# Kernel optimization log

Measured on AMD Instinct MI355X. Metric: run time of the kernel, lower is better.

Reference implementation:

```python
import jax, jax.numpy as jnp
import numpy as np

N_NODES = 10000

def _gcn_norm(edges, n_nodes):
    # PyG GCNConv default: add self-loops, symmetric normalization D^-1/2 A_hat D^-1/2
    src, dst = edges[0], edges[1]
    loop = jnp.arange(n_nodes, dtype=src.dtype)
    src = jnp.concatenate([src, loop])
    dst = jnp.concatenate([dst, loop])
    deg = jax.ops.segment_sum(jnp.ones_like(dst, dtype=jnp.float32), dst, num_segments=n_nodes)
    dinv = jnp.where(deg > 0, jax.lax.rsqrt(deg), 0.0)
    norm = dinv[src] * dinv[dst]  # [E + N]
    return src, dst, norm

def _gcn_layer(x, src, dst, norm, W, b):
    # linear transform, then gather -> weight -> scatter-add aggregation
    x = x @ W  # [N, F]
    msg = x[src] * norm[:, None]  # [E+N, F]
    out = jax.ops.segment_sum(msg, dst, num_segments=x.shape[0])
    return out + b

def setup_inputs() -> dict:
    key = jax.random.key(0)
    k1, k2, k3, k4 = jax.random.split(key, 4)
    d = 128
    E = 640000
    scale = 1.0 / np.sqrt(d)
    return {
        "nodes_embeddings": jax.random.normal(k1, (N_NODES, d), dtype=jnp.float32),
        "edges": jax.random.randint(k2, (2, E), 0, N_NODES, dtype=jnp.int64),
        "W1": jax.random.normal(k3, (d, d), dtype=jnp.float32) * scale,
        "b1": jnp.zeros((d,), dtype=jnp.float32),
        "W2": jax.random.normal(k4, (d, d), dtype=jnp.float32) * scale,
        "b2": jnp.zeros((d,), dtype=jnp.float32),
    }

def reference(nodes_embeddings, edges, W1, b1, W2, b2):
    src, dst, norm = _gcn_norm(edges, nodes_embeddings.shape[0])
    x = _gcn_layer(nodes_embeddings, src, dst, norm, W1, b1)
    x = _gcn_layer(x, src, dst, norm, W2, b2)
    return x
```

## Files before the change

kernel.cpp:

```cpp
#include <hip/hip_runtime.h>
#include <hip/hip_bf16.h>

#define D 128
#define NBINS 157
#define BIN_CAP 5120
#define EPB 4096

__device__ __forceinline__ unsigned rne_bf16(float f) {
    unsigned u = __float_as_uint(f);
    return (u + 0x7FFFu + ((u >> 16) & 1u)) >> 16;
}
__device__ __forceinline__ float bf16_lo(unsigned u) { return __uint_as_float(u << 16); }
__device__ __forceinline__ float bf16_hi(unsigned u) { return __uint_as_float(u & 0xFFFF0000u); }

__global__ __launch_bounds__(512) void fused_gemm_scatter(
        const float* __restrict__ X, const float* __restrict__ W,
        float* __restrict__ Y,
        const int* __restrict__ src, const int* __restrict__ dst,
        int* __restrict__ binTotal, int* __restrict__ binned,
        int E, int N, int gGemm) {
    __shared__ float smem[D * D];
    int tid = threadIdx.x;

    if ((int)blockIdx.x < gGemm) {
        {
            const float4* W4 = (const float4*)W;
            float4* Ws4 = (float4*)smem;
            #pragma unroll
            for (int i = 0; i < 8; ++i)
                Ws4[tid + 512 * i] = W4[tid + 512 * i];
        }
        __syncthreads();
        const float2* Ws2 = (const float2*)smem;
        int col2 = tid & 63;
        int wv   = __builtin_amdgcn_readfirstlane(tid >> 6);
        int row0 = blockIdx.x * 32 + wv * 4;
        if (row0 >= N) return;

        const float4* xr[4];
        #pragma unroll
        for (int r = 0; r < 4; ++r) {
            int rr = row0 + r; if (rr > N - 1) rr = N - 1;
            xr[r] = (const float4*)(X + (size_t)rr * D);
        }
        float accx[4] = {0.f, 0.f, 0.f, 0.f};
        float accy[4] = {0.f, 0.f, 0.f, 0.f};
        #pragma unroll 8
        for (int kb = 0; kb < 32; ++kb) {
            float4 xv[4];
            #pragma unroll
            for (int r = 0; r < 4; ++r) xv[r] = xr[r][kb];
            #pragma unroll
            for (int kk = 0; kk < 4; ++kk) {
                float2 w = Ws2[(4 * kb + kk) * 64 + col2];
                #pragma unroll
                for (int r = 0; r < 4; ++r) {
                    float xs = ((const float*)&xv[r])[kk];
                    accx[r] = fmaf(xs, w.x, accx[r]);
                    accy[r] = fmaf(xs, w.y, accy[r]);
                }
            }
        }
        #pragma unroll
        for (int r = 0; r < 4; ++r) {
            int rr = row0 + r;
            if (rr < N)
                ((float2*)Y)[(size_t)rr * 64 + col2] = make_float2(accx[r], accy[r]);
        }
    } else {
        int* cnt   = (int*)smem;
        int* loff  = cnt + 160;
        int* gbase = cnt + 320;
        int* scur  = cnt + 480;
        int* stage = cnt + 640;
        for (int b = tid; b < NBINS; b += 512) cnt[b] = 0;
        __syncthreads();

        int bid = blockIdx.x - gGemm;
        int base = bid * EPB + tid * 8;
        int s[8], dl[8], bn[8];
        int ne = 0;
        if (base + 8 <= E) {
            const int4* s4 = (const int4*)(src + base);
            const int4* d4 = (const int4*)(dst + base);
            int4 a0 = s4[0], a1 = s4[1], c0 = d4[0], c1 = d4[1];
            int ss[8] = {a0.x, a0.y, a0.z, a0.w, a1.x, a1.y, a1.z, a1.w};
            int dd[8] = {c0.x, c0.y, c0.z, c0.w, c1.x, c1.y, c1.z, c1.w};
            ne = 8;
            #pragma unroll
            for (int i = 0; i < 8; ++i) { s[i] = ss[i]; bn[i] = dd[i] >> 6; dl[i] = dd[i] & 63; }
        } else {
            for (int i = 0; i < 8; ++i) {
                int e = base + i;
                if (e < E) { s[ne] = src[e]; int d = dst[e]; bn[ne] = d >> 6; dl[ne] = d & 63; ++ne; }
            }
        }
        for (int i = 0; i < ne; ++i) atomicAdd(&cnt[bn[i]], 1);
        __syncthreads();

        if (tid < NBINS) gbase[tid] = atomicAdd(&binTotal[tid], cnt[tid]);
        if (tid < 64) {
            int c0 = (3 * tid     < NBINS) ? cnt[3 * tid    ] : 0;
            int c1 = (3 * tid + 1 < NBINS) ? cnt[3 * tid + 1] : 0;
            int c2 = (3 * tid + 2 < NBINS) ? cnt[3 * tid + 2] : 0;
            int tsum = c0 + c1 + c2;
            int incl = tsum;
            #pragma unroll
            for (int off = 1; off < 64; off <<= 1) {
                int t = __shfl_up(incl, off);
                if (tid >= off) incl += t;
            }
            int excl = incl - tsum;
            if (3 * tid     < NBINS) loff[3 * tid    ] = excl;
            if (3 * tid + 1 < NBINS) loff[3 * tid + 1] = excl + c0;
            if (3 * tid + 2 < NBINS) loff[3 * tid + 2] = excl + c0 + c1;
        }
        __syncthreads();
        if (tid < NBINS) scur[tid] = loff[tid];
        __syncthreads();

        for (int i = 0; i < ne; ++i) {
            int p = atomicAdd(&scur[bn[i]], 1);
            stage[p] = s[i] | (dl[i] << 14);
        }
        __syncthreads();

        int wv = tid >> 6, lane = tid & 63;
        for (int b = wv; b < NBINS; b += 8) {
            int n = cnt[b], so = loff[b], go = b * BIN_CAP + gbase[b];
            for (int i = lane; i < n; i += 64) binned[go + i] = stage[so + i];
        }
    }
}

__global__ __launch_bounds__(256) void sort_bins(const int* __restrict__ binTotal,
                                                 const int* __restrict__ binned,
                                                 unsigned short* __restrict__ csr16,
                                                 float* __restrict__ dinv,
                                                 int* __restrict__ nodeStart,
                                                 int* __restrict__ nodeEnd,
                                                 const float* __restrict__ Y,
                                                 unsigned* __restrict__ Zb,
                                                 unsigned* __restrict__ Zb2, int N) {
    __shared__ int h[4][64];
    __shared__ int cur[4][64];
    __shared__ float sdinv[64];
    __shared__ int padTot;
    __shared__ int stage[BIN_CAP];
    int b = blockIdx.x, tid = threadIdx.x;
    int wv = tid >> 6, lane = tid & 63;
    int cntb = binTotal[b];
    h[wv][lane] = 0;
    __syncthreads();
    const int* bp = binned + b * BIN_CAP;
    for (int i = tid; i < cntb; i += 256) atomicAdd(&h[wv][bp[i] >> 14], 1);
    __syncthreads();
    if (tid < 64) {
        int d0 = h[0][tid], d1 = h[1][tid], d2 = h[2][tid], d3 = h[3][tid];
        int deg = d0 + d1 + d2 + d3;
        int pdeg = (deg + 7) & ~7;
        int incl = pdeg;
        #pragma unroll
        for (int off = 1; off < 64; off <<= 1) {
            int t = __shfl_up(incl, off);
            if (tid >= off) incl += t;
        }
        int excl = incl - pdeg;
        cur[0][tid] = excl;
        cur[1][tid] = excl + d0;
        cur[2][tid] = excl + d0 + d1;
        cur[3][tid] = excl + d0 + d1 + d2;
        float dv = rsqrtf((float)(deg + 1));
        sdinv[tid] = dv;
        if (tid == 63) padTot = incl;
        int node = b * 64 + tid;
        if (node < N) {
            dinv[node]      = dv;
            nodeStart[node] = b * BIN_CAP + excl;
            nodeEnd[node]   = b * BIN_CAP + excl + pdeg;
        }
    }
    __syncthreads();
    int cntPad = padTot;
    for (int i = tid; i < cntPad; i += 256) stage[i] = N;
    __syncthreads();
    for (int i = tid; i < cntb; i += 256) {
        int p = bp[i];
        int pos = atomicAdd(&cur[wv][p >> 14], 1);
        stage[pos] = p & 0x3FFF;
    }
    {
        const float4* Y4 = (const float4*)Y;
        uint2* Zb2v = (uint2*)Zb;
        #pragma unroll
        for (int i = 0; i < 8; ++i) {
            int idx = tid + 256 * i;
            int row = idx >> 5, c = idx & 31;
            int node = b * 64 + row;
            if (node < N) {
                float4 v = Y4[(size_t)node * 32 + c];
                float dv = sdinv[row];
                uint2 o;
                o.x = (rne_bf16(v.y * dv) << 16) | rne_bf16(v.x * dv);
                o.y = (rne_bf16(v.w * dv) << 16) | rne_bf16(v.z * dv);
                Zb2v[(size_t)node * 32 + c] = o;
            }
        }
    }
    if (b == 0 && tid < 64) {
        Zb [(size_t)N * 64 + tid] = 0u;
        Zb2[(size_t)N * 64 + tid] = 0u;
    }
    __syncthreads();
    unsigned short* bw = csr16 + b * BIN_CAP;
    for (int i = tid; i < cntPad; i += 256) bw[i] = (unsigned short)stage[i];
}

__global__ __launch_bounds__(256) void aggregate(const unsigned* __restrict__ Zb,
                                                 const int* __restrict__ nodeStart,
                                                 const int* __restrict__ nodeEnd,
                                                 const unsigned short* __restrict__ csr16,
                                                 const float* __restrict__ dinv,
                                                 const float* __restrict__ bias,
                                                 float* __restrict__ Out, int N,
                                                 const float* __restrict__ W2,
                                                 unsigned* __restrict__ Zout) {
    __shared__ float rowsLds[8][128];
    const bool fused = (W2 != nullptr);
    int wv    = __builtin_amdgcn_readfirstlane(threadIdx.x >> 6);
    int nodeA = blockIdx.x * 8 + wv * 2;
    bool active = (nodeA < N);
    if (!fused && !active) return;
    int lane = threadIdx.x & 63;
    int l16  = lane & 15;

    if (active) {
        int nodeB = nodeA + 1;
        bool hasB = (nodeB < N);
        int g = lane >> 4;

        const uint4* Z4 = (const uint4*)Zb;
        float a0=0.f,a1=0.f,a2=0.f,a3=0.f,a4=0.f,a5=0.f,a6=0.f,a7=0.f;
        float b0=0.f,b1v=0.f,b2v=0.f,b3=0.f,b4v=0.f,b5=0.f,b6=0.f,b7=0.f;

        int eA = nodeStart[nodeA], endA = nodeEnd[nodeA];
        int eB = 0, endB = 0;
        if (hasB) { eB = nodeStart[nodeB]; endB = nodeEnd[nodeB]; }

        while (eA < endA || eB < endB) {
            int remA = endA - eA; int cntA = remA > 64 ? 64 : (remA > 0 ? remA : 0);
            int remB = endB - eB; int cntB = remB > 64 ? 64 : (remB > 0 ? remB : 0);
            int myA = (lane < cntA) ? (int)csr16[eA + lane] : N;
            int myB = (lane < cntB) ? (int)csr16[eB + lane] : N;
            int cmax = cntA > cntB ? cntA : cntB;
            int rounds = cmax >> 2;
            #pragma unroll 16
            for (int j = 0; j < rounds; ++j) {
                int idxA = __shfl(myA, j * 4 + g);
                int idxB = __shfl(myB, j * 4 + g);
                uint4 ua = Z4[idxA * 16 + l16];
                uint4 ub = Z4[idxB * 16 + l16];
                a0 += bf16_lo(ua.x); a1 += bf16_hi(ua.x);
                a2 += bf16_lo(ua.y); a3 += bf16_hi(ua.y);
                a4 += bf16_lo(ua.z); a5 += bf16_hi(ua.z);
                a6 += bf16_lo(ua.w); a7 += bf16_hi(ua.w);
                b0  += bf16_lo(ub.x); b1v += bf16_hi(ub.x);
                b2v += bf16_lo(ub.y); b3  += bf16_hi(ub.y);
                b4v += bf16_lo(ub.z); b5  += bf16_hi(ub.z);
                b6  += bf16_lo(ub.w); b7  += bf16_hi(ub.w);
            }
            eA += cntA; eB += cntB;
        }
        #pragma unroll
        for (int m = 16; m <= 32; m <<= 1) {
            a0 += __shfl_xor(a0, m); a1 += __shfl_xor(a1, m);
            a2 += __shfl_xor(a2, m); a3 += __shfl_xor(a3, m);
            a4 += __shfl_xor(a4, m); a5 += __shfl_xor(a5, m);
            a6 += __shfl_xor(a6, m); a7 += __shfl_xor(a7, m);
            b0  += __shfl_xor(b0, m);  b1v += __shfl_xor(b1v, m);
            b2v += __shfl_xor(b2v, m); b3  += __shfl_xor(b3, m);
            b4v += __shfl_xor(b4v, m); b5  += __shfl_xor(b5, m);
            b6  += __shfl_xor(b6, m);  b7  += __shfl_xor(b7, m);
        }
        int half = lane >> 4;
        if (half == 0 || (half == 1 && hasB)) {
            int node = half ? nodeB : nodeA;
            float r0 = half ? b0  : a0, r1 = half ? b1v : a1;
            float r2 = half ? b2v : a2, r3 = half ? b3  : a3;
            float r4 = half ? b4v : a4, r5 = half ? b5  : a5;
            float r6 = half ? b6  : a6, r7 = half ? b7  : a7;
            uint4 su = Z4[node * 16 + l16];
            float dv = dinv[node];
            const float4* bp4 = (const float4*)bias;
            float4 ba = bp4[l16 * 2], bb = bp4[l16 * 2 + 1];
            float4 o0, o1;
            o0.x = (r0 + bf16_lo(su.x)) * dv + ba.x;
            o0.y = (r1 + bf16_hi(su.x)) * dv + ba.y;
            o0.z = (r2 + bf16_lo(su.y)) * dv + ba.z;
            o0.w = (r3 + bf16_hi(su.y)) * dv + ba.w;
            o1.x = (r4 + bf16_lo(su.z)) * dv + bb.x;
            o1.y = (r5 + bf16_hi(su.z)) * dv + bb.y;
            o1.z = (r6 + bf16_lo(su.w)) * dv + bb.z;
            o1.w = (r7 + bf16_hi(su.w)) * dv + bb.w;
            if (fused) {
                float4* rp = (float4*)&rowsLds[wv * 2 + half][0];
                rp[l16 * 2]     = o0;
                rp[l16 * 2 + 1] = o1;
            } else {
                float4* op = (float4*)Out + (size_t)node * 32 + l16 * 2;
                op[0] = o0;
                op[1] = o1;
            }
        }
    }

    if (fused) {
        __syncthreads();
        int tid  = threadIdx.x;
        int colg = (tid & 31) << 2;
        int r    = tid >> 5;
        int node = blockIdx.x * 8 + r;
        const float* xrow = &rowsLds[r][0];
        float ac0 = 0.f, ac1 = 0.f, ac2 = 0.f, ac3 = 0.f;
        #pragma unroll 8
        for (int k = 0; k < 128; ++k) {
            float xs = xrow[k];
            float4 w4 = *(const float4*)(W2 + (size_t)k * D + colg);
            ac0 = fmaf(xs, w4.x, ac0);
            ac1 = fmaf(xs, w4.y, ac1);
            ac2 = fmaf(xs, w4.z, ac2);
            ac3 = fmaf(xs, w4.w, ac3);
        }
        if (node < N) {
            float dv = dinv[node];
            uint2 o;
            o.x = (rne_bf16(ac1 * dv) << 16) | rne_bf16(ac0 * dv);
            o.y = (rne_bf16(ac3 * dv) << 16) | rne_bf16(ac2 * dv);
            ((uint2*)Zout)[(size_t)node * 32 + (colg >> 2)] = o;
        }
    }
}

extern "C" void kernel_launch(void* const* d_in, const int* in_sizes, int n_in,
                              void* d_out, int out_size, void* d_ws, size_t ws_size,
                              hipStream_t stream) {
    const float* X  = (const float*)d_in[0];
    const int*   ed = (const int*)d_in[1];
    const float* W1 = (const float*)d_in[2];
    const float* b1 = (const float*)d_in[3];
    const float* W2 = (const float*)d_in[4];
    const float* b2 = (const float*)d_in[5];
    float* out = (float*)d_out;

    const int N = in_sizes[0] / D;
    const int E = in_sizes[1] / 2;
    const int* src = ed;
    const int* dst = ed + E;

    char* w = (char*)d_ws;
    float*    Y        = (float*)w;            w += (size_t)N * D * sizeof(float);
    unsigned* Zb       = (unsigned*)w;         w += (size_t)(N + 1) * 64 * sizeof(unsigned);
    unsigned* Zb2      = (unsigned*)w;         w += (size_t)(N + 1) * 64 * sizeof(unsigned);
    int*      binned   = (int*)w;              w += (size_t)NBINS * BIN_CAP * sizeof(int);
    unsigned short* csr16 = (unsigned short*)w; w += (size_t)NBINS * BIN_CAP * sizeof(unsigned short);
    float*    dinv     = (float*)w;            w += (size_t)N * sizeof(float);
    int*      nodeStart= (int*)w;              w += (size_t)N * sizeof(int);
    int*      nodeEnd  = (int*)w;              w += (size_t)N * sizeof(int);
    int*      binTotal = (int*)w;              w += (size_t)NBINS * sizeof(int);

    hipMemsetAsync(binTotal, 0, NBINS * sizeof(int), stream);

    int gGemm1 = (N + 31) / 32;
    int gScat  = (E + EPB - 1) / EPB;
    fused_gemm_scatter<<<gGemm1 + gScat, 512, 0, stream>>>(
        X, W1, Y, src, dst, binTotal, binned, E, N, gGemm1);
    sort_bins<<<NBINS, 256, 0, stream>>>(binTotal, binned, csr16, dinv,
                                         nodeStart, nodeEnd, Y, Zb, Zb2, N);

    int gAgg = (N + 7) / 8;
    aggregate<<<gAgg, 256, 0, stream>>>(Zb, nodeStart, nodeEnd, csr16, dinv,
                                        b1, out, N, W2, Zb2);
    aggregate<<<gAgg, 256, 0, stream>>>(Zb2, nodeStart, nodeEnd, csr16, dinv,
                                        b2, out, N, nullptr, nullptr);
}
```

Before: 140.8 us.

## Replace binned two-pass sort with degree count, scan, and atomic CSR scatter

CSR construction changes from shared-memory binning followed by a per-bin sort into three steps. Per-node degrees are counted with global atomics inside the GEMM kernel, a per-bin scan sets node offsets and cursors, and a new kernel scatters source indices into the CSR through global atomics on the per-node cursors. This drops the intermediate binned buffer and the sort pass, at the cost of many contended global atomics and an extra kernel launch. Node degrees are no longer padded to a multiple of 8, so the aggregate loop now rounds up its trip count and relies on lanes past the end reading the zero row N.

Measured after the change: 199.8 us. 1.42x slower.

```diff
diff --git a/kernel.cpp b/kernel.cpp
--- a/kernel.cpp
+++ b/kernel.cpp
@@ -13,11 +13,10 @@
 __device__ __forceinline__ float bf16_lo(unsigned u) { return __uint_as_float(u << 16); }
 __device__ __forceinline__ float bf16_hi(unsigned u) { return __uint_as_float(u & 0xFFFF0000u); }
 
-__global__ __launch_bounds__(512) void fused_gemm_scatter(
+__global__ __launch_bounds__(512) void fused_gemm_degcount(
         const float* __restrict__ X, const float* __restrict__ W,
         float* __restrict__ Y,
-        const int* __restrict__ src, const int* __restrict__ dst,
-        int* __restrict__ binTotal, int* __restrict__ binned,
+        const int* __restrict__ dst, int* __restrict__ deg,
         int E, int N, int gGemm) {
     __shared__ float smem[D * D];
     int tid = threadIdx.x;
@@ -68,130 +67,57 @@
                 ((float2*)Y)[(size_t)rr * 64 + col2] = make_float2(accx[r], accy[r]);
         }
     } else {
-        int* cnt   = (int*)smem;
-        int* loff  = cnt + 160;
-        int* gbase = cnt + 320;
-        int* scur  = cnt + 480;
-        int* stage = cnt + 640;
-        for (int b = tid; b < NBINS; b += 512) cnt[b] = 0;
-        __syncthreads();
-
         int bid = blockIdx.x - gGemm;
         int base = bid * EPB + tid * 8;
-        int s[8], dl[8], bn[8];
-        int ne = 0;
         if (base + 8 <= E) {
-            const int4* s4 = (const int4*)(src + base);
             const int4* d4 = (const int4*)(dst + base);
-            int4 a0 = s4[0], a1 = s4[1], c0 = d4[0], c1 = d4[1];
-            int ss[8] = {a0.x, a0.y, a0.z, a0.w, a1.x, a1.y, a1.z, a1.w};
-            int dd[8] = {c0.x, c0.y, c0.z, c0.w, c1.x, c1.y, c1.z, c1.w};
-            ne = 8;
-            #pragma unroll
-            for (int i = 0; i < 8; ++i) { s[i] = ss[i]; bn[i] = dd[i] >> 6; dl[i] = dd[i] & 63; }
+            int4 c0 = d4[0], c1 = d4[1];
+            atomicAdd(&deg[c0.x], 1); atomicAdd(&deg[c0.y], 1);
+            atomicAdd(&deg[c0.z], 1); atomicAdd(&deg[c0.w], 1);
+            atomicAdd(&deg[c1.x], 1); atomicAdd(&deg[c1.y], 1);
+            atomicAdd(&deg[c1.z], 1); atomicAdd(&deg[c1.w], 1);
         } else {
             for (int i = 0; i < 8; ++i) {
                 int e = base + i;
-                if (e < E) { s[ne] = src[e]; int d = dst[e]; bn[ne] = d >> 6; dl[ne] = d & 63; ++ne; }
-            }
-        }
-        for (int i = 0; i < ne; ++i) atomicAdd(&cnt[bn[i]], 1);
-        __syncthreads();
-
-        if (tid < NBINS) gbase[tid] = atomicAdd(&binTotal[tid], cnt[tid]);
-        if (tid < 64) {
-            int c0 = (3 * tid     < NBINS) ? cnt[3 * tid    ] : 0;
-            int c1 = (3 * tid + 1 < NBINS) ? cnt[3 * tid + 1] : 0;
-            int c2 = (3 * tid + 2 < NBINS) ? cnt[3 * tid + 2] : 0;
-            int tsum = c0 + c1 + c2;
-            int incl = tsum;
-            #pragma unroll
-            for (int off = 1; off < 64; off <<= 1) {
-                int t = __shfl_up(incl, off);
-                if (tid >= off) incl += t;
-            }
-            int excl = incl - tsum;
-            if (3 * tid     < NBINS) loff[3 * tid    ] = excl;
-            if (3 * tid + 1 < NBINS) loff[3 * tid + 1] = excl + c0;
-            if (3 * tid + 2 < NBINS) loff[3 * tid + 2] = excl + c0 + c1;
-        }
-        __syncthreads();
-        if (tid < NBINS) scur[tid] = loff[tid];
-        __syncthreads();
-
-        for (int i = 0; i < ne; ++i) {
-            int p = atomicAdd(&scur[bn[i]], 1);
-            stage[p] = s[i] | (dl[i] << 14);
-        }
-        __syncthreads();
-
-        int wv = tid >> 6, lane = tid & 63;
-        for (int b = wv; b < NBINS; b += 8) {
-            int n = cnt[b], so = loff[b], go = b * BIN_CAP + gbase[b];
-            for (int i = lane; i < n; i += 64) binned[go + i] = stage[so + i];
-        }
-    }
-}
-
-__global__ __launch_bounds__(256) void sort_bins(const int* __restrict__ binTotal,
-                                                 const int* __restrict__ binned,
-                                                 unsigned short* __restrict__ csr16,
-                                                 float* __restrict__ dinv,
-                                                 int* __restrict__ nodeStart,
-                                                 int* __restrict__ nodeEnd,
-                                                 const float* __restrict__ Y,
-                                                 unsigned* __restrict__ Zb,
-                                                 unsigned* __restrict__ Zb2, int N) {
-    __shared__ int h[4][64];
-    __shared__ int cur[4][64];
+                if (e < E) atomicAdd(&deg[dst[e]], 1);
+            }
+        }
+    }
+}
+
+__global__ __launch_bounds__(256) void scan_convert(
+        const int* __restrict__ deg,
+        float* __restrict__ dinv,
+        int* __restrict__ nodeStart, int* __restrict__ nodeEnd,
+        int* __restrict__ cursor,
+        const float* __restrict__ Y,
+        unsigned* __restrict__ Zb, unsigned* __restrict__ Zb2, int N) {
     __shared__ float sdinv[64];
-    __shared__ int padTot;
-    __shared__ int stage[BIN_CAP];
     int b = blockIdx.x, tid = threadIdx.x;
-    int wv = tid >> 6, lane = tid & 63;
-    int cntb = binTotal[b];
-    h[wv][lane] = 0;
-    __syncthreads();
-    const int* bp = binned + b * BIN_CAP;
-    for (int i = tid; i < cntb; i += 256) atomicAdd(&h[wv][bp[i] >> 14], 1);
-    __syncthreads();
     if (tid < 64) {
-        int d0 = h[0][tid], d1 = h[1][tid], d2 = h[2][tid], d3 = h[3][tid];
-        int deg = d0 + d1 + d2 + d3;
-        int pdeg = (deg + 7) & ~7;
-        int incl = pdeg;
+        int node = b * 64 + tid;
+        int dg = (node < N) ? deg[node] : 0;
+        int incl = dg;
         #pragma unroll
         for (int off = 1; off < 64; off <<= 1) {
             int t = __shfl_up(incl, off);
             if (tid >= off) incl += t;
         }
-        int excl = incl - pdeg;
-        cur[0][tid] = excl;
-        cur[1][tid] = excl + d0;
-        cur[2][tid] = excl + d0 + d1;
-        cur[3][tid] = excl + d0 + d1 + d2;
-        float dv = rsqrtf((float)(deg + 1));
+        int excl = incl - dg;
+        float dv = rsqrtf((float)(dg + 1));
         sdinv[tid] = dv;
-        if (tid == 63) padTot = incl;
-        int node = b * 64 + tid;
         if (node < N) {
+            int st = b * BIN_CAP + excl;
             dinv[node]      = dv;
-            nodeStart[node] = b * BIN_CAP + excl;
-            nodeEnd[node]   = b * BIN_CAP + excl + pdeg;
+            nodeStart[node] = st;
+            nodeEnd[node]   = st + dg;
+            cursor[node]    = st;
         }
     }
     __syncthreads();
-    int cntPad = padTot;
-    for (int i = tid; i < cntPad; i += 256) stage[i] = N;
-    __syncthreads();
-    for (int i = tid; i < cntb; i += 256) {
-        int p = bp[i];
-        int pos = atomicAdd(&cur[wv][p >> 14], 1);
-        stage[pos] = p & 0x3FFF;
-    }
     {
         const float4* Y4 = (const float4*)Y;
-        uint2* Zb2v = (uint2*)Zb;
+        uint2* Zp = (uint2*)Zb;
         #pragma unroll
         for (int i = 0; i < 8; ++i) {
             int idx = tid + 256 * i;
@@ -203,7 +129,7 @@
                 uint2 o;
                 o.x = (rne_bf16(v.y * dv) << 16) | rne_bf16(v.x * dv);
                 o.y = (rne_bf16(v.w * dv) << 16) | rne_bf16(v.z * dv);
-                Zb2v[(size_t)node * 32 + c] = o;
+                Zp[(size_t)node * 32 + c] = o;
             }
         }
     }
@@ -211,9 +137,32 @@
         Zb [(size_t)N * 64 + tid] = 0u;
         Zb2[(size_t)N * 64 + tid] = 0u;
     }
-    __syncthreads();
-    unsigned short* bw = csr16 + b * BIN_CAP;
-    for (int i = tid; i < cntPad; i += 256) bw[i] = (unsigned short)stage[i];
+}
+
+__global__ __launch_bounds__(512) void scatter_csr(
+        const int* __restrict__ src, const int* __restrict__ dst,
+        int* __restrict__ cursor, unsigned short* __restrict__ csr16, int E) {
+    int base = blockIdx.x * EPB + threadIdx.x * 8;
+    if (base + 8 <= E) {
+        const int4* s4 = (const int4*)(src + base);
+        const int4* d4 = (const int4*)(dst + base);
+        int4 a0 = s4[0], a1 = s4[1], c0 = d4[0], c1 = d4[1];
+        int ss[8] = {a0.x, a0.y, a0.z, a0.w, a1.x, a1.y, a1.z, a1.w};
+        int dd[8] = {c0.x, c0.y, c0.z, c0.w, c1.x, c1.y, c1.z, c1.w};
+        #pragma unroll
+        for (int i = 0; i < 8; ++i) {
+            int p = atomicAdd(&cursor[dd[i]], 1);
+            csr16[p] = (unsigned short)ss[i];
+        }
+    } else {
+        for (int i = 0; i < 8; ++i) {
+            int e = base + i;
+            if (e < E) {
+                int p = atomicAdd(&cursor[dst[e]], 1);
+                csr16[p] = (unsigned short)src[e];
+            }
+        }
+    }
 }
 
 __global__ __launch_bounds__(256) void aggregate(const unsigned* __restrict__ Zb,
@@ -253,7 +202,7 @@
             int myA = (lane < cntA) ? (int)csr16[eA + lane] : N;
             int myB = (lane < cntB) ? (int)csr16[eB + lane] : N;
             int cmax = cntA > cntB ? cntA : cntB;
-            int rounds = cmax >> 2;
+            int rounds = (cmax + 3) >> 2;
             #pragma unroll 16
             for (int j = 0; j < rounds; ++j) {
                 int idxA = __shfl(myA, j * 4 + g);
@@ -361,21 +310,22 @@
     float*    Y        = (float*)w;            w += (size_t)N * D * sizeof(float);
     unsigned* Zb       = (unsigned*)w;         w += (size_t)(N + 1) * 64 * sizeof(unsigned);
     unsigned* Zb2      = (unsigned*)w;         w += (size_t)(N + 1) * 64 * sizeof(unsigned);
-    int*      binned   = (int*)w;              w += (size_t)NBINS * BIN_CAP * sizeof(int);
     unsigned short* csr16 = (unsigned short*)w; w += (size_t)NBINS * BIN_CAP * sizeof(unsigned short);
     float*    dinv     = (float*)w;            w += (size_t)N * sizeof(float);
     int*      nodeStart= (int*)w;              w += (size_t)N * sizeof(int);
     int*      nodeEnd  = (int*)w;              w += (size_t)N * sizeof(int);
-    int*      binTotal = (int*)w;              w += (size_t)NBINS * sizeof(int);
-
-    hipMemsetAsync(binTotal, 0, NBINS * sizeof(int), stream);
+    int*      deg      = (int*)w;              w += (size_t)N * sizeof(int);
+    int*      cursor   = (int*)w;              w += (size_t)N * sizeof(int);
+
+    hipMemsetAsync(deg, 0, (size_t)N * sizeof(int), stream);
 
     int gGemm1 = (N + 31) / 32;
     int gScat  = (E + EPB - 1) / EPB;
-    fused_gemm_scatter<<<gGemm1 + gScat, 512, 0, stream>>>(
-        X, W1, Y, src, dst, binTotal, binned, E, N, gGemm1);
-    sort_bins<<<NBINS, 256, 0, stream>>>(binTotal, binned, csr16, dinv,
-                                         nodeStart, nodeEnd, Y, Zb, Zb2, N);
+    fused_gemm_degcount<<<gGemm1 + gScat, 512, 0, stream>>>(
+        X, W1, Y, dst, deg, E, N, gGemm1);
+    scan_convert<<<NBINS, 256, 0, stream>>>(deg, dinv, nodeStart, nodeEnd,
+                                            cursor, Y, Zb, Zb2, N);
+    scatter_csr<<<gScat, 512, 0, stream>>>(src, dst, cursor, csr16, E);
 
     int gAgg = (N + 7) / 8;
     aggregate<<<gAgg, 256, 0, stream>>>(Zb, nodeStart, nodeEnd, csr16, dinv,
```
